# Kernel tuning notes

Measured on AMD Instinct MI355X. Metric: run time of the kernel, lower is better.

Reference implementation:

```python
import jax, jax.numpy as jnp
import numpy as np

BN_EPS = 1e-5
NORM_EPS = 1e-12  # F.normalize default eps


def reference(x, conv_w, bn_gamma, bn_beta):
    # 1x1 conv dimension reduction: [B,2048,H,W] -> [B,256,H,W]
    z = jnp.einsum('bchw,dc->bdhw', x, conv_w)
    # BatchNorm2d (training-mode batch statistics) + ReLU
    mu = z.mean(axis=(0, 2, 3), keepdims=True)
    var = z.var(axis=(0, 2, 3), keepdims=True)
    z = (z - mu) / jnp.sqrt(var + BN_EPS)
    z = z * bn_gamma.reshape(1, -1, 1, 1) + bn_beta.reshape(1, -1, 1, 1)
    z = jax.nn.relu(z)

    B, d, h, w = z.shape
    M = h * w
    xm = z.reshape(B, d, M)
    # Covpool: y = x I_hat x^T with I_hat = (I - 11^T/M)/M == centered 2nd moment
    xc = xm - xm.mean(axis=-1, keepdims=True)
    cov = jnp.einsum('bdm,bem->bde', xc, xc) / M  # [B,d,d]

    # Eigen decomposition (cov is symmetric PSD; SVD of PSD == eigh)
    s, U = jnp.linalg.eigh(cov)  # s: [B,d], U: [B,d,d]
    eps = jnp.finfo(cov.dtype).eps
    s = jnp.maximum(s, eps)

    # ExponentialInverse: U exp(-S) U^T
    inv_x = jnp.einsum('bid,bd,bjd->bij', U, jnp.exp(-s), U)
    # Power (matrix sqrt): U S^{1/2} U^T
    out = jnp.einsum('bid,bd,bjd->bij', U, jnp.sqrt(s), U)

    # attention = out @ inv_x^T  (inv_x is symmetric, transpose kept for fidelity)
    att = jnp.einsum('bij,bkj->bik', out, inv_x)
    flat = att.reshape(B, -1)
    nrm = jnp.maximum(jnp.linalg.norm(flat, axis=1, keepdims=True), NORM_EPS)
    normalized = (flat / nrm).reshape(att.shape)
    att = out * (att / normalized)

    y = att + out
    iu = jnp.triu_indices(d)
    return y[:, iu[0], iu[1]]  # [B, d*(d+1)/2]


def setup_inputs() -> dict:
    key = jax.random.key(0)
    k1, k2 = jax.random.split(key)
    x = jax.random.normal(k1, (32, 2048, 28, 28), dtype=jnp.float32)
    # kaiming-normal fan_out scaling for 1x1 conv: std = sqrt(2/fan_out)=sqrt(2/256)
    conv_w = jax.random.normal(k2, (256, 2048), dtype=jnp.float32) * np.sqrt(2.0 / 256.0)
    bn_gamma = jnp.ones((256,), dtype=jnp.float32)
    bn_beta = jnp.zeros((256,), dtype=jnp.float32)
    return {'x': x, 'conv_w': conv_w, 'bn_gamma': bn_gamma, 'bn_beta': bn_beta}
```

## Files before the change

kernel.cpp:

```cpp
#include <hip/hip_runtime.h>


typedef unsigned short u16;
typedef __attribute__((ext_vector_type(8))) short bf16x8;
typedef __attribute__((ext_vector_type(4))) float f32x4;

__device__ __forceinline__ u16 f2bf(float f) {
  unsigned u = __builtin_bit_cast(unsigned, f);
  u += 0x7FFFu + ((u >> 16) & 1u);
  return (u16)(u >> 16);
}
__device__ __forceinline__ float bf2f(u16 h) {
  unsigned u = ((unsigned)h) << 16;
  return __builtin_bit_cast(float, u);
}

template<int MB>
__global__ __launch_bounds__(512)
void fuseN64_k(const u16* __restrict__ A0, const u16* __restrict__ B0, u16* __restrict__ C0,
               float al0, float b10, float dg0, const float* __restrict__ cf0,
               const u16* __restrict__ A1, const u16* __restrict__ B1, u16* __restrict__ C1,
               u16* __restrict__ D1, float al1, float b11, float dg1,
               float hc1, float hc2, float hc3, const float* __restrict__ cf1, long LO)
{
  __shared__ u16 ldsA[2][128][8][8];
  __shared__ u16 ldsB[2][64][8][8];
  int z = blockIdx.z;
  const bool hB = (z >= 32);
  const u16 *Ah, *Bh; u16 *C, *D = nullptr;
  float al, b1, dg; const float* cf;
  if (!hB) { Ah = A0; Bh = B0; C = C0; al = al0; b1 = b10; dg = dg0; cf = cf0; }
  else { z -= 32; Ah = A1; Bh = B1; C = C1; D = D1; al = al1; b1 = b11; dg = dg1; cf = cf1; }
  const long boff = (long)z * 65536;
  const int row0 = blockIdx.y * 128, col0 = blockIdx.x * 64;
  const int tid = threadIdx.x;
  const int wave = tid >> 6, lane = tid & 63;
  const int wm = wave >> 1, wn = wave & 1;
  const int mL = lane & 15, q = lane >> 4;
  const u16* baseA[2] = {Ah + boff, Ah + LO + boff};
  const u16* baseB[2] = {Bh + boff, Bh + LO + boff};

  f32x4 acc[2][2];
#pragma unroll
  for (int i = 0; i < 2; ++i)
#pragma unroll
    for (int j = 0; j < 2; ++j) acc[i][j] = {0.f, 0.f, 0.f, 0.f};

  for (int k0 = 0; k0 < 256; k0 += 64) {
    __syncthreads();
#pragma unroll
    for (int it = 0; it < 4; ++it) {
      const int t = it >> 1;
      const int r = ((it & 1) << 9) + tid;
      const int m = r >> 3, c = r & 7;
      *reinterpret_cast<uint4*>(&ldsA[t][m][c ^ (m & 7)][0]) =
          *reinterpret_cast<const uint4*>(baseA[t] + (long)(row0 + m) * 256 + k0 + c * 8);
    }
#pragma unroll
    for (int it = 0; it < 2; ++it) {
      const int m = tid >> 3, c = tid & 7;
      *reinterpret_cast<uint4*>(&ldsB[it][m][c ^ (m & 7)][0]) =
          *reinterpret_cast<const uint4*>(baseB[it] + (long)(col0 + m) * 256 + k0 + c * 8);
    }
    __syncthreads();
#pragma unroll
    for (int kk = 0; kk < 2; ++kk) {
      bf16x8 ah[2], alo[2], bh[2], bl[2];
#pragma unroll
      for (int i = 0; i < 2; ++i) {
        const int ma = wm * 32 + i * 16 + mL;
        const int ca = (kk * 4 + q) ^ (ma & 7);
        ah[i]  = *reinterpret_cast<const bf16x8*>(&ldsA[0][ma][ca][0]);
        alo[i] = *reinterpret_cast<const bf16x8*>(&ldsA[1][ma][ca][0]);
      }
#pragma unroll
      for (int j = 0; j < 2; ++j) {
        const int nb = wn * 32 + j * 16 + mL;
        const int cb = (kk * 4 + q) ^ (nb & 7);
        bh[j] = *reinterpret_cast<const bf16x8*>(&ldsB[0][nb][cb][0]);
        bl[j] = *reinterpret_cast<const bf16x8*>(&ldsB[1][nb][cb][0]);
      }
#pragma unroll
      for (int i = 0; i < 2; ++i)
#pragma unroll
        for (int j = 0; j < 2; ++j) {
          acc[i][j] = __builtin_amdgcn_mfma_f32_16x16x32_bf16(ah[i],  bh[j], acc[i][j], 0, 0, 0);
          acc[i][j] = __builtin_amdgcn_mfma_f32_16x16x32_bf16(ah[i],  bl[j], acc[i][j], 0, 0, 0);
          acc[i][j] = __builtin_amdgcn_mfma_f32_16x16x32_bf16(alo[i], bh[j], acc[i][j], 0, 0, 0);
        }
    }
  }

#pragma unroll
  for (int i = 0; i < 2; ++i) {
    const int rbase = row0 + wm * 32 + i * 16 + q * 4;
#pragma unroll
    for (int j = 0; j < 2; ++j) {
      const int cc = col0 + wn * 32 + j * 16 + mL;
#pragma unroll
      for (int rg = 0; rg < 4; ++rg) {
        const int rr = rbase + rg;
        const long o = boff + (long)rr * 256 + cc;
        const float vr = acc[i][j][rg];
        if (MB == 1 && hB) {
          u16 h = f2bf(vr);
          C[o] = h; C[o + LO] = f2bf(vr - bf2f(h));
          float hv = fmaf(vr, hc1, cf[o] * hc2);
          if (rr == cc) hv += hc3;
          h = f2bf(hv);
          D[o] = h; D[o + LO] = f2bf(hv - bf2f(h));
        } else {
          float v = al * vr;
          if (cf) v = fmaf(b1, cf[o], v);
          if (rr == cc) v += dg;
          const u16 h = f2bf(v);
          C[o] = h; C[o + LO] = f2bf(v - bf2f(h));
        }
      }
    }
  }
}

template<int MODE>
__global__ __launch_bounds__(512)
void gemmN64_k(const u16* __restrict__ Ah, const u16* __restrict__ Al,
               const u16* __restrict__ Bh, const u16* __restrict__ Bl,
               u16* __restrict__ Ch, u16* __restrict__ Cl,
               const float* __restrict__ cf, float alpha, float b1, float diag,
               float* __restrict__ attn2)
{
  __shared__ u16 ldsA[2][128][8][8];
  __shared__ u16 ldsB[2][64][8][8];
  const long boff = (long)blockIdx.z * 65536;
  const int row0 = blockIdx.y * 128, col0 = blockIdx.x * 64;
  const int tid = threadIdx.x;
  const int wave = tid >> 6, lane = tid & 63;
  const int wm = wave >> 1, wn = wave & 1;
  const int mL = lane & 15, q = lane >> 4;
  const u16* baseA[2] = {Ah + boff, Al + boff};
  const u16* baseB[2] = {Bh + boff, Bl + boff};

  f32x4 acc[2][2];
#pragma unroll
  for (int i = 0; i < 2; ++i)
#pragma unroll
    for (int j = 0; j < 2; ++j) acc[i][j] = {0.f, 0.f, 0.f, 0.f};

  for (int k0 = 0; k0 < 256; k0 += 64) {
    __syncthreads();
#pragma unroll
    for (int it = 0; it < 4; ++it) {
      const int t = it >> 1;
      const int r = ((it & 1) << 9) + tid;
      const int m = r >> 3, c = r & 7;
      *reinterpret_cast<uint4*>(&ldsA[t][m][c ^ (m & 7)][0]) =
          *reinterpret_cast<const uint4*>(baseA[t] + (long)(row0 + m) * 256 + k0 + c * 8);
    }
#pragma unroll
    for (int it = 0; it < 2; ++it) {
      const int m = tid >> 3, c = tid & 7;
      *reinterpret_cast<uint4*>(&ldsB[it][m][c ^ (m & 7)][0]) =
          *reinterpret_cast<const uint4*>(baseB[it] + (long)(col0 + m) * 256 + k0 + c * 8);
    }
    __syncthreads();
#pragma unroll
    for (int kk = 0; kk < 2; ++kk) {
      bf16x8 ah[2], alo[2], bh[2], bl[2];
#pragma unroll
      for (int i = 0; i < 2; ++i) {
        const int ma = wm * 32 + i * 16 + mL;
        const int ca = (kk * 4 + q) ^ (ma & 7);
        ah[i]  = *reinterpret_cast<const bf16x8*>(&ldsA[0][ma][ca][0]);
        alo[i] = *reinterpret_cast<const bf16x8*>(&ldsA[1][ma][ca][0]);
      }
#pragma unroll
      for (int j = 0; j < 2; ++j) {
        const int nb = wn * 32 + j * 16 + mL;
        const int cb = (kk * 4 + q) ^ (nb & 7);
        bh[j] = *reinterpret_cast<const bf16x8*>(&ldsB[0][nb][cb][0]);
        bl[j] = *reinterpret_cast<const bf16x8*>(&ldsB[1][nb][cb][0]);
      }
#pragma unroll
      for (int i = 0; i < 2; ++i)
#pragma unroll
        for (int j = 0; j < 2; ++j) {
          acc[i][j] = __builtin_amdgcn_mfma_f32_16x16x32_bf16(ah[i],  bh[j], acc[i][j], 0, 0, 0);
          acc[i][j] = __builtin_amdgcn_mfma_f32_16x16x32_bf16(ah[i],  bl[j], acc[i][j], 0, 0, 0);
          acc[i][j] = __builtin_amdgcn_mfma_f32_16x16x32_bf16(alo[i], bh[j], acc[i][j], 0, 0, 0);
        }
    }
  }

  if (MODE == 2) {
    float ssum = 0.f;
#pragma unroll
    for (int i = 0; i < 2; ++i)
#pragma unroll
      for (int j = 0; j < 2; ++j)
#pragma unroll
        for (int rg = 0; rg < 4; ++rg) ssum = fmaf(acc[i][j][rg], acc[i][j][rg], ssum);
#pragma unroll
    for (int o = 32; o > 0; o >>= 1) ssum += __shfl_down(ssum, o);
    __syncthreads();
    float* red = (float*)&ldsA[0][0][0][0];
    if (lane == 0) red[wave] = ssum;
    __syncthreads();
    if (tid == 0) {
      float t8 = 0.f;
#pragma unroll
      for (int wv = 0; wv < 8; ++wv) t8 += red[wv];
      atomicAdd(attn2 + blockIdx.z, t8);
    }
    return;
  }

#pragma unroll
  for (int i = 0; i < 2; ++i) {
    const int rbase = row0 + wm * 32 + i * 16 + q * 4;
#pragma unroll
    for (int j = 0; j < 2; ++j) {
      const int cc = col0 + wn * 32 + j * 16 + mL;
#pragma unroll
      for (int rg = 0; rg < 4; ++rg) {
        const int rr = rbase + rg;
        const long o = boff + (long)rr * 256 + cc;
        float v = alpha * acc[i][j][rg];
        if (cf) v = fmaf(b1, cf[o], v);
        if (rr == cc) v += diag;
        const u16 h = f2bf(v);
        Ch[o] = h; Cl[o] = f2bf(v - bf2f(h));
      }
    }
  }
}

__global__ __launch_bounds__(512)
void conv_k(const u16* __restrict__ wb, const float* __restrict__ x,
            float* __restrict__ z0, float* __restrict__ z1)
{
  __shared__ u16 ldsA[256][8][8];
  __shared__ u16 ldsB[64][8][8];
  const int tid = threadIdx.x;
  const int b = blockIdx.z;
  const int n0 = blockIdx.x * 64;
  const int kb0 = blockIdx.y * 1024;
  const int wave = tid >> 6, lane = tid & 63;
  const int wm = wave >> 1, wn = wave & 1;
  const int mL = lane & 15, q = lane >> 4;
  const float* xb = x + (long)b * 2048 * 784;
  float* zp = (blockIdx.y == 0 ? z0 : z1);

  f32x4 acc[4][2];
#pragma unroll
  for (int i = 0; i < 4; ++i)
#pragma unroll
    for (int j = 0; j < 2; ++j) acc[i][j] = {0.f, 0.f, 0.f, 0.f};

  const int kc = tid >> 6, nc = tid & 63;
  const int gn = n0 + nc;
  const bool nok = (gn < 784);
  const int ch = kc ^ (nc & 7);

  auto GATHER = [&](int kg, float* v) {
    const float* ps = xb + (long)(kg + kc * 8) * 784 + gn;
#pragma unroll
    for (int jk = 0; jk < 8; ++jk) v[jk] = nok ? ps[(long)jk * 784] : 0.f;
  };
  auto STAGEA = [&](int kg) {
#pragma unroll
    for (int it = 0; it < 4; ++it) {
      const int g = it * 512 + tid;
      const int m = g >> 3, c = g & 7;
      *reinterpret_cast<uint4*>(&ldsA[m][c ^ (m & 7)][0]) =
          *reinterpret_cast<const uint4*>(wb + (long)m * 2048 + kg + c * 8);
    }
  };
  auto WRITEB = [&](const float* v) {
    ushort4 ua, ub;
    ua.x = f2bf(v[0]); ua.y = f2bf(v[1]); ua.z = f2bf(v[2]); ua.w = f2bf(v[3]);
    ub.x = f2bf(v[4]); ub.y = f2bf(v[5]); ub.z = f2bf(v[6]); ub.w = f2bf(v[7]);
    *reinterpret_cast<ushort4*>(&ldsB[nc][ch][0]) = ua;
    *reinterpret_cast<ushort4*>(&ldsB[nc][ch][4]) = ub;
  };
  auto DOMFMA = [&]() {
#pragma unroll
    for (int kk = 0; kk < 2; ++kk) {
      bf16x8 af[4], bfv[2];
#pragma unroll
      for (int i = 0; i < 4; ++i) {
        const int ma = wm * 64 + i * 16 + mL;
        af[i] = *reinterpret_cast<const bf16x8*>(&ldsA[ma][(kk * 4 + q) ^ (ma & 7)][0]);
      }
#pragma unroll
      for (int j = 0; j < 2; ++j) {
        const int nb = wn * 32 + j * 16 + mL;
        bfv[j] = *reinterpret_cast<const bf16x8*>(&ldsB[nb][(kk * 4 + q) ^ (nb & 7)][0]);
      }
#pragma unroll
      for (int i = 0; i < 4; ++i)
#pragma unroll
        for (int j = 0; j < 2; ++j)
          acc[i][j] = __builtin_amdgcn_mfma_f32_16x16x32_bf16(af[i], bfv[j], acc[i][j], 0, 0, 0);
    }
  };

  float va[8], vb2[8];
  GATHER(kb0, va);
  for (int k0 = 0; k0 < 1024; k0 += 128) {
    __syncthreads();
    STAGEA(kb0 + k0);
    WRITEB(va);
    __syncthreads();
    GATHER(kb0 + k0 + 64, vb2);
    DOMFMA();
    __syncthreads();
    STAGEA(kb0 + k0 + 64);
    WRITEB(vb2);
    __syncthreads();
    if (k0 + 128 < 1024) GATHER(kb0 + k0 + 128, va);
    DOMFMA();
  }

#pragma unroll
  for (int i = 0; i < 4; ++i) {
    const int rbase = wm * 64 + i * 16 + q * 4;
#pragma unroll
    for (int j = 0; j < 2; ++j) {
      const int cc = n0 + wn * 32 + j * 16 + mL;
      if (cc >= 784) continue;
#pragma unroll
      for (int rg = 0; rg < 4; ++rg)
        zp[((long)b * 256 + rbase + rg) * 784 + cc] = acc[i][j][rg];
    }
  }
}

__global__ __launch_bounds__(512)
void gram_k(const u16* __restrict__ zb, const float* __restrict__ rs,
            float* __restrict__ cov, u16* __restrict__ C2h, u16* __restrict__ C2l)
{
  __shared__ u16 ldsA[128][8][8];
  __shared__ u16 ldsB[64][8][8];
  const int tid = threadIdx.x;
  const int b = blockIdx.z;
  const int col0 = blockIdx.x * 64, row0 = blockIdx.y * 128;
  const int wave = tid >> 6, lane = tid & 63;
  const int wm = wave >> 1, wn = wave & 1;
  const int mL = lane & 15, q = lane >> 4;
  const u16* zbb = zb + (long)b * 256 * 832;

  f32x4 acc[2][2];
#pragma unroll
  for (int i = 0; i < 2; ++i)
#pragma unroll
    for (int j = 0; j < 2; ++j) acc[i][j] = {0.f, 0.f, 0.f, 0.f};

  for (int k0 = 0; k0 < 832; k0 += 64) {
    __syncthreads();
#pragma unroll
    for (int it = 0; it < 2; ++it) {
      const int r = it * 512 + tid;
      const int m = r >> 3, c = r & 7;
      *reinterpret_cast<uint4*>(&ldsA[m][c ^ (m & 7)][0]) =
          *reinterpret_cast<const uint4*>(zbb + (long)(row0 + m) * 832 + k0 + c * 8);
    }
    {
      const int m = tid >> 3, c = tid & 7;
      *reinterpret_cast<uint4*>(&ldsB[m][c ^ (m & 7)][0]) =
          *reinterpret_cast<const uint4*>(zbb + (long)(col0 + m) * 832 + k0 + c * 8);
    }
    __syncthreads();
#pragma unroll
    for (int kk = 0; kk < 2; ++kk) {
      bf16x8 af[2], bfv[2];
#pragma unroll
      for (int i = 0; i < 2; ++i) {
        const int ma = wm * 32 + i * 16 + mL;
        af[i] = *reinterpret_cast<const bf16x8*>(&ldsA[ma][(kk * 4 + q) ^ (ma & 7)][0]);
      }
#pragma unroll
      for (int j = 0; j < 2; ++j) {
        const int nb = wn * 32 + j * 16 + mL;
        bfv[j] = *reinterpret_cast<const bf16x8*>(&ldsB[nb][(kk * 4 + q) ^ (nb & 7)][0]);
      }
#pragma unroll
      for (int i = 0; i < 2; ++i)
#pragma unroll
        for (int j = 0; j < 2; ++j)
          acc[i][j] = __builtin_amdgcn_mfma_f32_16x16x32_bf16(af[i], bfv[j], acc[i][j], 0, 0, 0);
    }
  }
  const float inv_m = 1.f / 784.f;
#pragma unroll
  for (int i = 0; i < 2; ++i) {
    const int rr0 = row0 + wm * 32 + i * 16 + q * 4;
#pragma unroll
    for (int j = 0; j < 2; ++j) {
      const int cc = col0 + wn * 32 + j * 16 + mL;
      const float mu_c = rs[b * 256 + cc] * inv_m;
#pragma unroll
      for (int rg = 0; rg < 4; ++rg) {
        const int rr = rr0 + rg;
        const float mu_r = rs[b * 256 + rr] * inv_m;
        const long o = ((long)b * 256 + rr) * 256 + cc;
        const float cv = fmaf(acc[i][j][rg], inv_m, -mu_r * mu_c);
        cov[o] = cv;
        const u16 h = f2bf(cv);
        C2h[o] = h; C2l[o] = f2bf(cv - bf2f(h));
      }
    }
  }
}

__global__ __launch_bounds__(256)
void bn_stats_k(const float* __restrict__ z0, const float* __restrict__ z1,
                float* __restrict__ ps, float* __restrict__ pq)
{
  const int d = blockIdx.x, sl = blockIdx.y, t = threadIdx.x;
  const int lane = t & 63, wid = t >> 6;
  __shared__ float ws[4], wq[4];
  float s = 0.f, qq = 0.f;
  for (int b = sl * 4; b < sl * 4 + 4; ++b) {
    const long off = ((long)b * 256 + d) * 784;
    for (int q4 = t; q4 < 196; q4 += 256) {
      const float4 a = *reinterpret_cast<const float4*>(z0 + off + q4 * 4);
      const float4 c = *reinterpret_cast<const float4*>(z1 + off + q4 * 4);
      const float v0 = a.x + c.x, v1 = a.y + c.y, v2 = a.z + c.z, v3 = a.w + c.w;
      s += v0 + v1 + v2 + v3;
      qq = fmaf(v0, v0, fmaf(v1, v1, fmaf(v2, v2, fmaf(v3, v3, qq))));
    }
  }
#pragma unroll
  for (int o = 32; o > 0; o >>= 1) { s += __shfl_down(s, o); qq += __shfl_down(qq, o); }
  if (lane == 0) { ws[wid] = s; wq[wid] = qq; }
  __syncthreads();
  if (t == 0) {
    ps[d * 8 + sl] = ws[0] + ws[1] + ws[2] + ws[3];
    pq[d * 8 + sl] = wq[0] + wq[1] + wq[2] + wq[3];
  }
}

__global__ __launch_bounds__(256)
void bn_apply_k(const float* __restrict__ z0, const float* __restrict__ z1,
                const float* __restrict__ gamma, const float* __restrict__ beta,
                const float* __restrict__ ps, const float* __restrict__ pq,
                u16* __restrict__ zb, float* __restrict__ rs)
{
  const int d = blockIdx.x, b = blockIdx.y, t = threadIdx.x;
  const int lane = t & 63, wid = t >> 6;
  __shared__ float bc[2], ws[4];
  if (t == 0) {
    float sum = 0.f, sq = 0.f;
#pragma unroll
    for (int s8 = 0; s8 < 8; ++s8) { sum += ps[d * 8 + s8]; sq += pq[d * 8 + s8]; }
    const float inv_n = 1.f / 25088.f;
    const float mean = sum * inv_n;
    const float var = sq * inv_n - mean * mean;
    const float sc = gamma[d] * rsqrtf(var + 1e-5f);
    bc[0] = sc; bc[1] = fmaf(-mean, sc, beta[d]);
  }
  __syncthreads();
  const float sc = bc[0], sh = bc[1];
  const long off = ((long)b * 256 + d) * 784;
  u16* qp = zb + ((long)b * 256 + d) * 832;
  float rsum = 0.f;
  for (int q4 = t; q4 < 208; q4 += 256) {
    ushort4 u = {0, 0, 0, 0};
    if (q4 < 196) {
      const float4 a = *reinterpret_cast<const float4*>(z0 + off + q4 * 4);
      const float4 c = *reinterpret_cast<const float4*>(z1 + off + q4 * 4);
      const float v0 = fmaxf(fmaf(a.x + c.x, sc, sh), 0.f);
      const float v1 = fmaxf(fmaf(a.y + c.y, sc, sh), 0.f);
      const float v2 = fmaxf(fmaf(a.z + c.z, sc, sh), 0.f);
      const float v3 = fmaxf(fmaf(a.w + c.w, sc, sh), 0.f);
      u.x = f2bf(v0); u.y = f2bf(v1); u.z = f2bf(v2); u.w = f2bf(v3);
      rsum += v0 + v1 + v2 + v3;
    }
    *reinterpret_cast<ushort4*>(qp + q4 * 4) = u;
  }
#pragma unroll
  for (int o = 32; o > 0; o >>= 1) rsum += __shfl_down(rsum, o);
  if (lane == 0) ws[wid] = rsum;
  __syncthreads();
  if (t == 0) rs[b * 256 + d] = ws[0] + ws[1] + ws[2] + ws[3];
}

__global__ __launch_bounds__(1024)
void power_k(const float* __restrict__ cov, float* __restrict__ s,
             float* __restrict__ attn2)
{
  const int b = blockIdx.x, tid = threadIdx.x;
  const int i = tid & 255, g = tid >> 8;
  const float* A = cov + (long)b * 65536;
  __shared__ float v[256];
  __shared__ float part[4][256];
  __shared__ float red[4];
  if (g == 0) v[i] = 1.f;
  __syncthreads();
  float lam = 1.f;
  for (int it = 0; it < 10; ++it) {
    float u = 0.f;
    const int jb = g * 64;
#pragma unroll 8
    for (int j = jb; j < jb + 64; ++j) u = fmaf(A[(long)j * 256 + i], v[j], u);
    part[g][i] = u;
    __syncthreads();
    if (g == 0) {
      u = part[0][i] + part[1][i] + part[2][i] + part[3][i];
      float ss = u * u;
#pragma unroll
      for (int o = 32; o > 0; o >>= 1) ss += __shfl_down(ss, o);
      if ((i & 63) == 0) red[i >> 6] = ss;
    }
    __syncthreads();
    lam = sqrtf(red[0] + red[1] + red[2] + red[3]);
    if (g == 0) v[i] = u / lam;
    __syncthreads();
  }
  if (tid == 0) { s[b] = 1.8f / lam; attn2[b] = 0.f; }
}

__global__ __launch_bounds__(256)
void init_k(const float* __restrict__ cov, const float* __restrict__ s,
            u16* __restrict__ Yh, u16* __restrict__ Yl,
            u16* __restrict__ Th, u16* __restrict__ Tl)
{
  const int b = blockIdx.y, i = blockIdx.x, j = threadIdx.x;
  const long o = ((long)b * 256 + i) * 256 + j;
  const float a = cov[o] * s[b];
  u16 h = f2bf(a);
  Yh[o] = h; Yl[o] = f2bf(a - bf2f(h));
  float tv = -0.5f * a;
  if (i == j) tv += 1.5f;
  h = f2bf(tv);
  Th[o] = h; Tl[o] = f2bf(tv - bf2f(h));
}

__global__ __launch_bounds__(256)
void out_k(const u16* __restrict__ Yh, const u16* __restrict__ Yl,
           const float* __restrict__ s, const float* __restrict__ attn2,
           float* __restrict__ out)
{
  const int i = blockIdx.x, b = blockIdx.y, j = threadIdx.x;
  if (j < i) return;
  const float inv = rsqrtf(s[b]);
  const float nrm = fmaxf(sqrtf(fmaxf(attn2[b], 0.f)) * inv, 1e-12f);
  const float scv = inv * (1.f + nrm);
  const long o = ((long)b * 256 + i) * 256 + j;
  const long off = (long)b * 32896 + (long)i * 256 - (long)i * (i - 1) / 2 + (j - i);
  out[off] = (bf2f(Yh[o]) + bf2f(Yl[o])) * scv;
}

__global__ __launch_bounds__(256)
void cast_w_k(const float* __restrict__ w, u16* __restrict__ wb)
{
  const int idx = blockIdx.x * 256 + threadIdx.x;
  wb[idx] = f2bf(w[idx]);
}

extern "C" void kernel_launch(void* const* d_in, const int* in_sizes, int n_in,
                              void* d_out, int out_size, void* d_ws, size_t ws_size,
                              hipStream_t stream)
{
  const float* x     = (const float*)d_in[0];
  const float* w     = (const float*)d_in[1];
  const float* gamma = (const float*)d_in[2];
  const float* beta  = (const float*)d_in[3];
  float* out = (float*)d_out;

  const long PS = 4194304;
  const long LO = 2097152;
  u16* S[9];
  for (int k = 0; k < 9; ++k) S[k] = (u16*)d_ws + (long)k * PS;
  char* base = (char*)d_ws;
  float* z0  = (float*)(base + 75497472);
  float* z1  = (float*)(base + 101187584);
  u16*   zb  = (u16*)(base + 126877696);
  float* cov = (float*)(base + 140509184);
  u16*   wbuf = (u16*)(base + 140509184);
  float* st  = (float*)(base + 148897792);
  float* sv = st, *attn2 = st + 32, *rs = st + 64;
  float* ps = st + 64 + 8192, *pq = ps + 2048;
  u16 *C2 = S[5], *V = S[6], *Ha = S[7], *Hb = S[8];

  const dim3 blk(256), blk5(512);
  const dim3 gF(4, 2, 64);
  const dim3 gT(4, 2, 32);
  const dim3 gE(256, 32);
  const float* nullf = nullptr;

  cast_w_k<<<dim3(2048), blk, 0, stream>>>(w, wbuf);
  conv_k<<<dim3(13, 2, 32), blk5, 0, stream>>>(wbuf, x, z0, z1);
  bn_stats_k<<<dim3(256, 8), blk, 0, stream>>>(z0, z1, ps, pq);
  bn_apply_k<<<dim3(256, 32), blk, 0, stream>>>(z0, z1, gamma, beta, ps, pq, zb, rs);
  gram_k<<<gT, blk5, 0, stream>>>(zb, rs, cov, C2, C2 + LO);
  power_k<<<dim3(32), dim3(1024), 0, stream>>>(cov, sv, attn2);
  init_k<<<gE, blk, 0, stream>>>(cov, sv, S[0], S[0] + LO, S[1], S[1] + LO);

  fuseN64_k<1><<<gF, blk5, 0, stream>>>(
      S[0], S[1], S[2], 1.f, 0.f, 0.f, nullf,
      C2, C2, V, Ha, 1.f, 0.f, 0.f,
      1.f / 40320.f, -1.f / 5040.f, 1.f / 720.f, cov, LO);

  int iY = 2, iZ = 1, fa = 0, fb = 3, fc = 4;
  for (int it = 1; it <= 7; ++it) {
    const int iT = fa;
    if (it == 1)
      fuseN64_k<0><<<gF, blk5, 0, stream>>>(
          S[iZ], S[iY], S[iT], -0.5f, 0.f, 1.5f, nullf,
          V, Ha, Hb, (u16*)nullptr, 1.f, -1.f / 120.f, 1.f / 24.f,
          0.f, 0.f, 0.f, cov, LO);
    else if (it == 2)
      fuseN64_k<0><<<gF, blk5, 0, stream>>>(
          S[iZ], S[iY], S[iT], -0.5f, 0.f, 1.5f, nullf,
          V, Hb, Ha, (u16*)nullptr, 1.f, -1.f / 6.f, 0.5f,
          0.f, 0.f, 0.f, cov, LO);
    else if (it == 3)
      fuseN64_k<0><<<gF, blk5, 0, stream>>>(
          S[iZ], S[iY], S[iT], -0.5f, 0.f, 1.5f, nullf,
          V, Ha, Hb, (u16*)nullptr, 1.f, -1.f, 1.f,
          0.f, 0.f, 0.f, cov, LO);
    else
      gemmN64_k<0><<<gT, blk5, 0, stream>>>(
          S[iZ], S[iZ] + LO, S[iY], S[iY] + LO, S[iT], S[iT] + LO,
          nullf, -0.5f, 0.f, 1.5f, (float*)nullptr);
    if (it < 7) {
      fuseN64_k<0><<<gF, blk5, 0, stream>>>(
          S[iY], S[iT], S[fb], 1.f, 0.f, 0.f, nullf,
          S[iT], S[iZ], S[fc], (u16*)nullptr, 1.f, 0.f, 0.f,
          0.f, 0.f, 0.f, nullf, LO);
      const int nY = fb, nZ = fc;
      fa = iY; fb = iZ; fc = iT;
      iY = nY; iZ = nZ;
    } else {
      gemmN64_k<0><<<gT, blk5, 0, stream>>>(
          S[iY], S[iY] + LO, S[iT], S[iT] + LO, S[fb], S[fb] + LO,
          nullf, 1.f, 0.f, 0.f, (float*)nullptr);
      iY = fb;
    }
  }

  gemmN64_k<2><<<gT, blk5, 0, stream>>>(
      S[iY], S[iY] + LO, Hb, Hb + LO, (u16*)nullptr, (u16*)nullptr,
      nullf, 1.f, 0.f, 0.f, attn2);
  out_k<<<gE, blk, 0, stream>>>(S[iY], S[iY] + LO, sv, attn2, out);
}
```

Measured before the change: 734.3 us.

## Split conv K four ways and warp-specialize A/B staging with float4 gathers

After: 670.5 us. -8.7%, faster.

```diff
diff --git a/kernel.cpp b/kernel.cpp
--- a/kernel.cpp
+++ b/kernel.cpp
@@ -236,19 +236,21 @@
 
 __global__ __launch_bounds__(512)
 void conv_k(const u16* __restrict__ wb, const float* __restrict__ x,
-            float* __restrict__ z0, float* __restrict__ z1)
+            float* __restrict__ z0, float* __restrict__ z1,
+            float* __restrict__ z2, float* __restrict__ z3)
 {
   __shared__ u16 ldsA[256][8][8];
-  __shared__ u16 ldsB[64][8][8];
+  __shared__ u16 ldsB[64][16][8];
   const int tid = threadIdx.x;
   const int b = blockIdx.z;
   const int n0 = blockIdx.x * 64;
-  const int kb0 = blockIdx.y * 1024;
+  const int kb0 = blockIdx.y * 512;
   const int wave = tid >> 6, lane = tid & 63;
   const int wm = wave >> 1, wn = wave & 1;
   const int mL = lane & 15, q = lane >> 4;
   const float* xb = x + (long)b * 2048 * 784;
-  float* zp = (blockIdx.y == 0 ? z0 : z1);
+  float* zp = (blockIdx.y == 0) ? z0 : (blockIdx.y == 1) ? z1
+            : (blockIdx.y == 2) ? z2 : z3;
 
   f32x4 acc[4][2];
 #pragma unroll
@@ -256,33 +258,45 @@
 #pragma unroll
     for (int j = 0; j < 2; ++j) acc[i][j] = {0.f, 0.f, 0.f, 0.f};
 
-  const int kc = tid >> 6, nc = tid & 63;
-  const int gn = n0 + nc;
-  const bool nok = (gn < 784);
-  const int ch = kc ^ (nc & 7);
-
-  auto GATHER = [&](int kg, float* v) {
-    const float* ps = xb + (long)(kg + kc * 8) * 784 + gn;
-#pragma unroll
-    for (int jk = 0; jk < 8; ++jk) v[jk] = nok ? ps[(long)jk * 784] : 0.f;
-  };
-  auto STAGEA = [&](int kg) {
-#pragma unroll
-    for (int it = 0; it < 4; ++it) {
-      const int g = it * 512 + tid;
-      const int m = g >> 3, c = g & 7;
-      *reinterpret_cast<uint4*>(&ldsA[m][c ^ (m & 7)][0]) =
-          *reinterpret_cast<const uint4*>(wb + (long)m * 2048 + kg + c * 8);
-    }
-  };
-  auto WRITEB = [&](const float* v) {
-    ushort4 ua, ub;
-    ua.x = f2bf(v[0]); ua.y = f2bf(v[1]); ua.z = f2bf(v[2]); ua.w = f2bf(v[3]);
-    ub.x = f2bf(v[4]); ub.y = f2bf(v[5]); ub.z = f2bf(v[6]); ub.w = f2bf(v[7]);
-    *reinterpret_cast<ushort4*>(&ldsB[nc][ch][0]) = ua;
-    *reinterpret_cast<ushort4*>(&ldsB[nc][ch][4]) = ub;
-  };
-  auto DOMFMA = [&]() {
+  const bool isB = (tid >= 256);
+  const int t2 = tid & 255;
+  const int o8 = t2 >> 4, nq = t2 & 15;
+  const int gnq = n0 + nq * 4;
+  const bool nok = (gnq < 784);
+
+  for (int ks = 0; ks < 4; ++ks) {
+    const int kg = kb0 + ks * 128;
+    __syncthreads();
+    if (!isB) {
+#pragma unroll
+      for (int it = 0; it < 8; ++it) {
+        const int g = it * 256 + t2;
+        const int m = g >> 3, c = g & 7;
+        *reinterpret_cast<uint4*>(&ldsA[m][c ^ (m & 7)][0]) =
+            *reinterpret_cast<const uint4*>(wb + (long)m * 2048 + kg + c * 8);
+      }
+    } else {
+      float4 f[8];
+#pragma unroll
+      for (int jk = 0; jk < 8; ++jk)
+        f[jk] = nok ? *reinterpret_cast<const float4*>(
+                          xb + (long)(kg + o8 * 8 + jk) * 784 + gnq)
+                    : make_float4(0.f, 0.f, 0.f, 0.f);
+      const float (*ff)[4] = reinterpret_cast<const float(*)[4]>(f);
+#pragma unroll
+      for (int j = 0; j < 4; ++j) {
+        const int n = nq * 4 + j;
+        const int ch = o8 ^ (n & 7);
+        ushort4 ua, ub;
+        ua.x = f2bf(ff[0][j]); ua.y = f2bf(ff[1][j]);
+        ua.z = f2bf(ff[2][j]); ua.w = f2bf(ff[3][j]);
+        ub.x = f2bf(ff[4][j]); ub.y = f2bf(ff[5][j]);
+        ub.z = f2bf(ff[6][j]); ub.w = f2bf(ff[7][j]);
+        *reinterpret_cast<ushort4*>(&ldsB[n][ch][0]) = ua;
+        *reinterpret_cast<ushort4*>(&ldsB[n][ch][4]) = ub;
+      }
+    }
+    __syncthreads();
 #pragma unroll
     for (int kk = 0; kk < 2; ++kk) {
       bf16x8 af[4], bfv[2];
@@ -302,23 +316,36 @@
         for (int j = 0; j < 2; ++j)
           acc[i][j] = __builtin_amdgcn_mfma_f32_16x16x32_bf16(af[i], bfv[j], acc[i][j], 0, 0, 0);
     }
-  };
-
-  float va[8], vb2[8];
-  GATHER(kb0, va);
-  for (int k0 = 0; k0 < 1024; k0 += 128) {
-    __syncthreads();
-    STAGEA(kb0 + k0);
-    WRITEB(va);
-    __syncthreads();
-    GATHER(kb0 + k0 + 64, vb2);
-    DOMFMA();
-    __syncthreads();
-    STAGEA(kb0 + k0 + 64);
-    WRITEB(vb2);
-    __syncthreads();
-    if (k0 + 128 < 1024) GATHER(kb0 + k0 + 128, va);
-    DOMFMA();
+    __syncthreads();
+    if (!isB) {
+#pragma unroll
+      for (int it = 0; it < 8; ++it) {
+        const int g = it * 256 + t2;
+        const int m = g >> 3, c = g & 7;
+        *reinterpret_cast<uint4*>(&ldsA[m][c ^ (m & 7)][0]) =
+            *reinterpret_cast<const uint4*>(wb + (long)m * 2048 + kg + 64 + c * 8);
+      }
+    }
+    __syncthreads();
+#pragma unroll
+    for (int kk = 0; kk < 2; ++kk) {
+      bf16x8 af[4], bfv[2];
+#pragma unroll
+      for (int i = 0; i < 4; ++i) {
+        const int ma = wm * 64 + i * 16 + mL;
+        af[i] = *reinterpret_cast<const bf16x8*>(&ldsA[ma][(kk * 4 + q) ^ (ma & 7)][0]);
+      }
+#pragma unroll
+      for (int j = 0; j < 2; ++j) {
+        const int nb = wn * 32 + j * 16 + mL;
+        bfv[j] = *reinterpret_cast<const bf16x8*>(&ldsB[nb][(8 + kk * 4 + q) ^ (nb & 7)][0]);
+      }
+#pragma unroll
+      for (int i = 0; i < 4; ++i)
+#pragma unroll
+        for (int j = 0; j < 2; ++j)
+          acc[i][j] = __builtin_amdgcn_mfma_f32_16x16x32_bf16(af[i], bfv[j], acc[i][j], 0, 0, 0);
+    }
   }
 
 #pragma unroll
@@ -414,6 +441,7 @@
 
 __global__ __launch_bounds__(256)
 void bn_stats_k(const float* __restrict__ z0, const float* __restrict__ z1,
+                const float* __restrict__ z2, const float* __restrict__ z3,
                 float* __restrict__ ps, float* __restrict__ pq)
 {
   const int d = blockIdx.x, sl = blockIdx.y, t = threadIdx.x;
@@ -423,9 +451,14 @@
   for (int b = sl * 4; b < sl * 4 + 4; ++b) {
     const long off = ((long)b * 256 + d) * 784;
     for (int q4 = t; q4 < 196; q4 += 256) {
-      const float4 a = *reinterpret_cast<const float4*>(z0 + off + q4 * 4);
-      const float4 c = *reinterpret_cast<const float4*>(z1 + off + q4 * 4);
-      const float v0 = a.x + c.x, v1 = a.y + c.y, v2 = a.z + c.z, v3 = a.w + c.w;
+      const float4 a0 = *reinterpret_cast<const float4*>(z0 + off + q4 * 4);
+      const float4 a1 = *reinterpret_cast<const float4*>(z1 + off + q4 * 4);
+      const float4 a2 = *reinterpret_cast<const float4*>(z2 + off + q4 * 4);
+      const float4 a3 = *reinterpret_cast<const float4*>(z3 + off + q4 * 4);
+      const float v0 = (a0.x + a1.x) + (a2.x + a3.x);
+      const float v1 = (a0.y + a1.y) + (a2.y + a3.y);
+      const float v2 = (a0.z + a1.z) + (a2.z + a3.z);
+      const float v3 = (a0.w + a1.w) + (a2.w + a3.w);
       s += v0 + v1 + v2 + v3;
       qq = fmaf(v0, v0, fmaf(v1, v1, fmaf(v2, v2, fmaf(v3, v3, qq))));
     }
@@ -442,6 +475,7 @@
 
 __global__ __launch_bounds__(256)
 void bn_apply_k(const float* __restrict__ z0, const float* __restrict__ z1,
+                const float* __restrict__ z2, const float* __restrict__ z3,
                 const float* __restrict__ gamma, const float* __restrict__ beta,
                 const float* __restrict__ ps, const float* __restrict__ pq,
                 u16* __restrict__ zb, float* __restrict__ rs)
@@ -467,12 +501,14 @@
   for (int q4 = t; q4 < 208; q4 += 256) {
     ushort4 u = {0, 0, 0, 0};
     if (q4 < 196) {
-      const float4 a = *reinterpret_cast<const float4*>(z0 + off + q4 * 4);
-      const float4 c = *reinterpret_cast<const float4*>(z1 + off + q4 * 4);
-      const float v0 = fmaxf(fmaf(a.x + c.x, sc, sh), 0.f);
-      const float v1 = fmaxf(fmaf(a.y + c.y, sc, sh), 0.f);
-      const float v2 = fmaxf(fmaf(a.z + c.z, sc, sh), 0.f);
-      const float v3 = fmaxf(fmaf(a.w + c.w, sc, sh), 0.f);
+      const float4 a0 = *reinterpret_cast<const float4*>(z0 + off + q4 * 4);
+      const float4 a1 = *reinterpret_cast<const float4*>(z1 + off + q4 * 4);
+      const float4 a2 = *reinterpret_cast<const float4*>(z2 + off + q4 * 4);
+      const float4 a3 = *reinterpret_cast<const float4*>(z3 + off + q4 * 4);
+      const float v0 = fmaxf(fmaf((a0.x + a1.x) + (a2.x + a3.x), sc, sh), 0.f);
+      const float v1 = fmaxf(fmaf((a0.y + a1.y) + (a2.y + a3.y), sc, sh), 0.f);
+      const float v2 = fmaxf(fmaf((a0.z + a1.z) + (a2.z + a3.z), sc, sh), 0.f);
+      const float v3 = fmaxf(fmaf((a0.w + a1.w) + (a2.w + a3.w), sc, sh), 0.f);
       u.x = f2bf(v0); u.y = f2bf(v1); u.z = f2bf(v2); u.w = f2bf(v3);
       rsum += v0 + v1 + v2 + v3;
     }
@@ -575,10 +611,12 @@
   char* base = (char*)d_ws;
   float* z0  = (float*)(base + 75497472);
   float* z1  = (float*)(base + 101187584);
-  u16*   zb  = (u16*)(base + 126877696);
-  float* cov = (float*)(base + 140509184);
-  u16*   wbuf = (u16*)(base + 140509184);
-  float* st  = (float*)(base + 148897792);
+  float* z2  = (float*)(base + 126877696);
+  float* z3  = (float*)(base + 152567808);
+  u16*   zb  = (u16*)(base + 178257920);
+  float* cov = (float*)(base + 191889408);
+  u16*   wbuf = (u16*)(base + 191889408);
+  float* st  = (float*)(base + 200278016);
   float* sv = st, *attn2 = st + 32, *rs = st + 64;
   float* ps = st + 64 + 8192, *pq = ps + 2048;
   u16 *C2 = S[5], *V = S[6], *Ha = S[7], *Hb = S[8];
@@ -590,9 +628,9 @@
   const float* nullf = nullptr;
 
   cast_w_k<<<dim3(2048), blk, 0, stream>>>(w, wbuf);
-  conv_k<<<dim3(13, 2, 32), blk5, 0, stream>>>(wbuf, x, z0, z1);
-  bn_stats_k<<<dim3(256, 8), blk, 0, stream>>>(z0, z1, ps, pq);
-  bn_apply_k<<<dim3(256, 32), blk, 0, stream>>>(z0, z1, gamma, beta, ps, pq, zb, rs);
+  conv_k<<<dim3(13, 4, 32), blk5, 0, stream>>>(wbuf, x, z0, z1, z2, z3);
+  bn_stats_k<<<dim3(256, 8), blk, 0, stream>>>(z0, z1, z2, z3, ps, pq);
+  bn_apply_k<<<dim3(256, 32), blk, 0, stream>>>(z0, z1, z2, z3, gamma, beta, ps, pq, zb, rs);
   gram_k<<<gT, blk5, 0, stream>>>(zb, rs, cov, C2, C2 + LO);
   power_k<<<dim3(32), dim3(1024), 0, stream>>>(cov, sv, attn2);
   init_k<<<gE, blk, 0, stream>>>(cov, sv, S[0], S[0] + LO, S[1], S[1] + LO);
```
